# Optimization experiments

Measured on AMD Instinct MI355X. Metric: run time of the kernel, lower is better.

Reference implementation:

```python
import jax, jax.numpy as jnp
import numpy as np

NI = 256  # channels (c)
EPS = 1e-5  # BatchNorm eps


def setup_inputs() -> dict:
    key = jax.random.key(0)
    ks = jax.random.split(key, 7)
    n, c, h, w = 8, NI, 96, 96
    inp = jax.random.normal(ks[0], (n, c, h, w), dtype=jnp.float32)
    bn_gamma = jnp.ones((c,), dtype=jnp.float32)
    bn_beta = jnp.zeros((c,), dtype=jnp.float32)
    s_qkv = 1.0 / np.sqrt(c)
    w_qkv = jax.random.uniform(ks[1], (c, 3 * c), dtype=jnp.float32, minval=-s_qkv, maxval=s_qkv)
    b_qkv = jax.random.uniform(ks[2], (3 * c,), dtype=jnp.float32, minval=-s_qkv, maxval=s_qkv)
    w_proj = jax.random.uniform(ks[3], (c, c), dtype=jnp.float32, minval=-s_qkv, maxval=s_qkv)
    b_proj = jax.random.uniform(ks[4], (c,), dtype=jnp.float32, minval=-s_qkv, maxval=s_qkv)
    return {"inp": inp, "bn_gamma": bn_gamma, "bn_beta": bn_beta,
            "w_qkv": w_qkv, "b_qkv": b_qkv, "w_proj": w_proj, "b_proj": b_proj}


def reference(inp, bn_gamma, bn_beta, w_qkv, b_qkv, w_proj, b_proj):
    n, c, h, w = inp.shape
    # BatchNorm2d (training-mode batch statistics, biased variance)
    mean = jnp.mean(inp, axis=(0, 2, 3), keepdims=True)
    var = jnp.var(inp, axis=(0, 2, 3), keepdims=True)
    xn = (inp - mean) * jax.lax.rsqrt(var + EPS)
    xn = xn * bn_gamma.reshape(1, c, 1, 1) + bn_beta.reshape(1, c, 1, 1)
    # (n, c, h*w) -> (n, s, c)
    x = jnp.transpose(xn.reshape(n, c, h * w), (0, 2, 1))
    # fused QKV projection: (n, s, 3c)
    qkv = x @ w_qkv + b_qkv
    q, k, v = jnp.split(qkv, 3, axis=-1)  # each (n, s, c); nheads=1
    # linear attention: v + q @ (k^T @ v), avoids the (s, s) score matrix
    kv = jnp.einsum('nsd,nse->nde', k, v)        # (n, c, c)
    attn = v + jnp.einsum('nsd,nde->nse', q, kv)  # (n, s, c)
    # output projection (dropout is identity in eval mode)
    y = attn @ w_proj + b_proj                    # (n, s, c)
    y = jnp.transpose(y, (0, 2, 1)).reshape(n, c, h, w)
    return y + inp
```

## Files before the change

kernel.cpp:

```cpp
#include <hip/hip_runtime.h>
#include <hip/hip_bf16.h>
#include <stdint.h>

#define S 9216
#define C 256
#define NB 8
#define EPS 1e-5f

typedef __attribute__((ext_vector_type(8))) short bf16x8;
typedef __attribute__((ext_vector_type(4))) float f32x4;
typedef unsigned short u16;
typedef unsigned int u32;

#define WS_SC   0
#define WS_RX   4096
#define WS_DS   16384
#define WS_U    20480
#define WS_PV2  32768
#define WS_P1   45056
#define WS_PW   49152
#define WS_SHW  53248
#define WS_CZ   57344
#define WS_WKT  65536
#define WS_WPT  196608
#define WS_WPV  327680
#define WS_GB   458752
#define WS_T1   1507328
#define WS_AC2  2555904
#define WS_M    3604480
#define WS_XB   5242880
#define WS_XBT  42991616
#define WS_P    80740352

__device__ __forceinline__ float bf2f(u16 b) { return __uint_as_float((u32)b << 16); }
__device__ __forceinline__ u16 cvt1(float x) {
    __hip_bfloat16 h = __float2bfloat16(x);
    return *(u16*)&h;
}
__device__ __forceinline__ bf16x8 pack8(float4 a, float4 b) {
    union { bf16x8 v; u16 h[8]; } u;
    u.h[0] = cvt1(a.x); u.h[1] = cvt1(a.y); u.h[2] = cvt1(a.z); u.h[3] = cvt1(a.w);
    u.h[4] = cvt1(b.x); u.h[5] = cvt1(b.y); u.h[6] = cvt1(b.z); u.h[7] = cvt1(b.w);
    return u.v;
}
__device__ __forceinline__ void gl16(const u16* g, u16* l) {
    __builtin_amdgcn_global_load_lds(
        (const __attribute__((address_space(1))) unsigned int*)g,
        (__attribute__((address_space(3))) unsigned int*)l, 16, 0, 0);
}

__global__ __launch_bounds__(256)
void wt_build(const float* __restrict__ w_qkv, const float* __restrict__ w_proj,
              u16* __restrict__ wkT, u16* __restrict__ wpT) {
    const int r0 = blockIdx.x, c = threadIdx.x;
    if (r0 < 256) {
        wkT[(size_t)r0 * 256 + c] = cvt1(w_qkv[(size_t)c * 768 + 256 + r0]);
    } else {
        const int o = r0 - 256;
        wpT[(size_t)o * 256 + c] = cvt1(w_proj[(size_t)c * 256 + o]);
    }
}

__global__ __launch_bounds__(256)
void wpv_gemm(const u16* __restrict__ wpT, const float* __restrict__ w_qkv,
              u16* __restrict__ Wpv) {
    const int bid = blockIdx.x;
    const int ot = bid >> 2, ct = bid & 3;
    const int tid = threadIdx.x;
    const int w = tid >> 6, l = tid & 63, g = l >> 4, r = l & 15;
    const int wr = w >> 1, wc = w & 1;
    const int mb = ot * 64 + wr * 32, nb = ct * 64 + wc * 32;

    f32x4 acc[2][2];
    #pragma unroll
    for (int i = 0; i < 2; ++i)
        #pragma unroll
        for (int j = 0; j < 2; ++j) acc[i][j] = (f32x4){0.f, 0.f, 0.f, 0.f};

    for (int k0 = 0; k0 < 256; k0 += 32) {
        bf16x8 a[2], b[2];
        #pragma unroll
        for (int i = 0; i < 2; ++i)
            a[i] = *(const bf16x8*)&wpT[(size_t)(mb + i * 16 + r) * 256 + k0 + g * 8];
        #pragma unroll
        for (int j = 0; j < 2; ++j) {
            const float* p = w_qkv + (size_t)(nb + j * 16 + r) * 768 + 512 + k0 + g * 8;
            b[j] = pack8(*(const float4*)p, *(const float4*)(p + 4));
        }
        #pragma unroll
        for (int i = 0; i < 2; ++i)
            #pragma unroll
            for (int j = 0; j < 2; ++j)
                acc[i][j] = __builtin_amdgcn_mfma_f32_16x16x32_bf16(a[i], b[j], acc[i][j], 0, 0, 0);
    }
    #pragma unroll
    for (int i = 0; i < 2; ++i)
        #pragma unroll
        for (int q = 0; q < 4; ++q) {
            const int row = mb + i * 16 + g * 4 + q;
            #pragma unroll
            for (int j = 0; j < 2; ++j)
                Wpv[(size_t)row * 256 + nb + j * 16 + r] = cvt1(acc[i][j][q]);
        }
}

__global__ __launch_bounds__(256)
void cvt(const float* __restrict__ inp, u16* __restrict__ xb, u16* __restrict__ xbT,
         float* __restrict__ rx, float* __restrict__ diagS) {
    __shared__ u32 T32[64 * 129];
    const int bid = blockIdx.x;
    const int z = bid / 144, sb = bid % 144;
    const int s0 = sb * 64;
    const int t = threadIdx.x;
    const int l = t & 63, w = t >> 6;
    const int s4 = (l & 15) * 4, rq = l >> 4;
    const int odd = rq & 1;

    #pragma unroll
    for (int half = 0; half < 2; ++half) {
        float4 v[8];
        #pragma unroll
        for (int it = 0; it < 8; ++it) {
            const int row = (half * 8 + it) * 16 + w * 4 + rq;
            v[it] = *(const float4*)&inp[((size_t)(z * C + row)) * S + s0 + s4];
        }
        #pragma unroll
        for (int it = 0; it < 8; ++it) {
            const int row = (half * 8 + it) * 16 + w * 4 + rq;
            const size_t gidx = ((size_t)(z * C + row)) * S + s0 + s4;
            u16 b0 = cvt1(v[it].x), b1 = cvt1(v[it].y), b2 = cvt1(v[it].z), b3 = cvt1(v[it].w);
            u32 m01 = (u32)b0 | ((u32)b1 << 16);
            u32 m23 = (u32)b2 | ((u32)b3 << 16);
            uint2 pk; pk.x = m01; pk.y = m23;
            *(uint2*)&xb[gidx] = pk;
            u32 p01 = (u32)__shfl_xor((int)m01, 16, 64);
            u32 p23 = (u32)__shfl_xor((int)m23, 16, 64);
            u32 wA, wB;
            if (!odd) {
                wA = (m01 & 0xffffu) | ((p01 & 0xffffu) << 16);
                wB = (m01 >> 16) | (p01 & 0xffff0000u);
            } else {
                wA = (p23 & 0xffffu) | ((m23 & 0xffffu) << 16);
                wB = (p23 >> 16) | (m23 & 0xffff0000u);
            }
            const int row2 = row >> 1;
            const int su = s4 + odd * 2;
            T32[(su + 0) * 129 + row2] = wA;
            T32[(su + 1) * 129 + row2] = wB;
        }
    }
    __syncthreads();
    {
        const int cw = t >> 1, hi = t & 1;
        float sum = 0.f, ssq = 0.f;
        #pragma unroll 8
        for (int s = 0; s < 64; ++s) {
            u32 wv = T32[s * 129 + cw];
            float v = bf2f(hi ? (u16)(wv >> 16) : (u16)(wv & 0xffffu));
            sum += v; ssq = fmaf(v, v, ssq);
        }
        atomicAdd(&rx[z * 256 + t], sum);
        atomicAdd(&diagS[t], ssq);
    }
    const int sl = t >> 2, q4 = t & 3;
    u16* dst = xbT + ((size_t)z * S + s0 + sl) * 256 + q4 * 64;
    const u32* Trow = &T32[sl * 129 + q4 * 32];
    #pragma unroll
    for (int kk = 0; kk < 8; ++kk) {
        const int c0 = (kk * 4 + q4 * 8) & 31;
        uint4 q;
        q.x = Trow[c0 + 0]; q.y = Trow[c0 + 1];
        q.z = Trow[c0 + 2]; q.w = Trow[c0 + 3];
        *(uint4*)&dst[c0 * 2] = q;
    }
}

__global__ __launch_bounds__(256)
void bn_fin(const float* __restrict__ diagS, const float* __restrict__ rx,
            const float* __restrict__ gamma, const float* __restrict__ beta,
            float* __restrict__ sc_sh) {
    const int c = threadIdx.x;
    float s = 0.f;
    #pragma unroll
    for (int z = 0; z < NB; ++z) s += rx[z * 256 + c];
    const float q = diagS[c];
    const float invN = 1.0f / (float)(NB * S);
    float m = s * invN;
    float var = q * invN - m * m;
    float rstd = rsqrtf(var + EPS);
    float sc = gamma[c] * rstd;
    sc_sh[c] = sc;
    sc_sh[C + c] = beta[c] - m * sc;
}

__global__ __launch_bounds__(256)
void gram(const u16* __restrict__ xb, float* __restrict__ P) {
    __shared__ u16 Asm[128 * 32];
    __shared__ u16 Bsm[128 * 32];
    const int bid = blockIdx.x;
    const int wid = (bid & 7) * 96 + (bid >> 3);
    const int z = wid / 96;
    const int rem = wid % 96;
    const int tile = rem >> 5;
    const int sp = rem & 31;
    const int ti = (tile == 1) ? 1 : 0;
    const int tj = (tile == 0) ? 0 : 1;
    const bool diag = (tile < 2);

    const int t = threadIdx.x;
    const int w = t >> 6, l = t & 63, g = l >> 4, r = l & 15;
    const int wr = w >> 1, wc = w & 1;
    const int rsub = l >> 2, csub = (l & 3) * 8;

    const u16* Az = xb + (size_t)z * C * S;

    f32x4 acc[4][4];
    #pragma unroll
    for (int i = 0; i < 4; ++i)
        #pragma unroll
        for (int j = 0; j < 4; ++j) acc[i][j] = (f32x4){0.f, 0.f, 0.f, 0.f};

    const int sbeg = sp * 288;
    for (int k0 = 0; k0 < 288; k0 += 32) {
        const int sc = sbeg + k0 + csub;
        #pragma unroll
        for (int q = 0; q < 2; ++q) {
            const int ii = w * 2 + q;
            const int row16 = ii * 16 + rsub;
            gl16(Az + (size_t)(ti * 128 + row16) * S + sc, &Asm[ii * 512]);
            if (!diag)
                gl16(Az + (size_t)(tj * 128 + row16) * S + sc, &Bsm[ii * 512]);
        }
        __syncthreads();
        const u16* Bb = diag ? Asm : Bsm;
        bf16x8 a[4], b[4];
        #pragma unroll
        for (int i = 0; i < 4; ++i)
            a[i] = *(const bf16x8*)&Asm[(wr * 64 + i * 16 + r) * 32 + g * 8];
        #pragma unroll
        for (int j = 0; j < 4; ++j)
            b[j] = *(const bf16x8*)&Bb[(wc * 64 + j * 16 + r) * 32 + g * 8];
        #pragma unroll
        for (int i = 0; i < 4; ++i)
            #pragma unroll
            for (int j = 0; j < 4; ++j)
                acc[i][j] = __builtin_amdgcn_mfma_f32_16x16x32_bf16(a[i], b[j], acc[i][j], 0, 0, 0);
        __syncthreads();
    }
    float* PP = P + (((size_t)(z * 3 + tile) * 32 + sp) << 14);
    #pragma unroll
    for (int i = 0; i < 4; ++i)
        #pragma unroll
        for (int q = 0; q < 4; ++q) {
            const int row = wr * 64 + i * 16 + g * 4 + q;
            #pragma unroll
            for (int j = 0; j < 4; ++j)
                PP[row * 128 + wc * 64 + j * 16 + r] = acc[i][j][q];
        }
}

__global__ __launch_bounds__(256)
void g_red(const float* __restrict__ P, const float* __restrict__ rx,
           const float* __restrict__ sc_sh, u16* __restrict__ Gb) {
    __shared__ float scs[256], shs[256], rxl[256];
    __shared__ u16 TT[8][132];
    const int bid = blockIdx.x;
    const int z = bid / 48;
    const int rem = bid % 48;
    const int tile = rem >> 4;
    const int rc = rem & 15;
    const int ti = (tile == 1) ? 1 : 0;
    const int tj = (tile == 0) ? 0 : 1;
    const int t = threadIdx.x;
    scs[t] = sc_sh[t]; shs[t] = sc_sh[C + t]; rxl[t] = rx[z * 256 + t];
    __syncthreads();
    const int col = t & 127;
    const int r0 = t >> 7;
    const float* Pbase = P + (((size_t)(z * 3 + tile) * 32) << 14) + rc * 8 * 128 + col;
    u16* Gz = Gb + (size_t)z * 65536;
    #pragma unroll
    for (int k = 0; k < 4; ++k) {
        const int rl = r0 + k * 2;
        float s = 0.f;
        #pragma unroll 4
        for (int sp = 0; sp < 32; ++sp)
            s += Pbase[((size_t)sp << 14) + rl * 128];
        const int gr = ti * 128 + rc * 8 + rl;
        const int gc = tj * 128 + col;
        float v = scs[gr] * scs[gc] * s + scs[gr] * shs[gc] * rxl[gr]
                + shs[gr] * scs[gc] * rxl[gc] + 9216.f * shs[gr] * shs[gc];
        u16 o = cvt1(v);
        Gz[(size_t)gr * 256 + gc] = o;
        TT[rl][col] = o;
    }
    if (ti != tj) {
        __syncthreads();
        if (t < 128) {
            const int gc = tj * 128 + t;
            u16 o8[8];
            #pragma unroll
            for (int rl = 0; rl < 8; ++rl) o8[rl] = TT[rl][t];
            *(uint4*)&Gz[(size_t)gc * 256 + ti * 128 + rc * 8] = *(uint4*)o8;
        }
    }
}

__global__ __launch_bounds__(256)
void prep_v(const float* __restrict__ sc_sh, const float* __restrict__ rx,
            const u16* __restrict__ wkT, const u16* __restrict__ Wpv,
            const u16* __restrict__ wpT, const float* __restrict__ w_qkv,
            const float* __restrict__ b_qkv,
            float* __restrict__ uvec, float* __restrict__ pvec,
            float* __restrict__ p1, float* __restrict__ pw, float* __restrict__ shw) {
    const int z = blockIdx.x, t = threadIdx.x;
    __shared__ float rsn[256], bvl[256], shl[256];
    rsn[t] = sc_sh[t] * rx[z * 256 + t] + 9216.f * sc_sh[C + t];
    bvl[t] = b_qkv[512 + t];
    shl[t] = sc_sh[C + t];
    __syncthreads();
    float au = 0.f, ap = 0.f, apw = 0.f;
    const u16* krow = wkT + (size_t)t * 256;
    const u16* prow = Wpv + (size_t)t * 256;
    for (int cb = 0; cb < 256; cb += 8) {
        uint4 kp = *(const uint4*)&krow[cb];
        uint4 pp = *(const uint4*)&prow[cb];
        const u16* kk = (const u16*)&kp;
        const u16* qq = (const u16*)&pp;
        #pragma unroll
        for (int u = 0; u < 8; ++u) {
            au = fmaf(bf2f(kk[u]), rsn[cb + u], au);
            float pv = bf2f(qq[u]);
            ap = fmaf(pv, rsn[cb + u], ap);
            apw = fmaf(pv, shl[cb + u], apw);
        }
    }
    uvec[z * 256 + t] = au;
    pvec[z * 256 + t] = ap;
    if (z == 0) {
        float a1 = 0.f, asw = 0.f;
        const u16* wrow = wpT + (size_t)t * 256;
        for (int cb = 0; cb < 256; cb += 8) {
            uint4 wp = *(const uint4*)&wrow[cb];
            const u16* ww = (const u16*)&wp;
            #pragma unroll
            for (int u = 0; u < 8; ++u) a1 = fmaf(bf2f(ww[u]), bvl[cb + u], a1);
        }
        for (int c = 0; c < 256; ++c)
            asw = fmaf(w_qkv[(size_t)c * 768 + t], shl[c], asw);
        p1[t] = a1;
        pw[t] = apw;
        shw[t] = asw;
    }
}

__global__ __launch_bounds__(256)
void t1_gemm(const u16* __restrict__ Wpv, const u16* __restrict__ Gb,
             u16* __restrict__ T1) {
    const int bid = blockIdx.x;
    const int wid = (bid & 7) * 16 + (bid >> 3);
    const int z = wid >> 4, ot = (wid >> 2) & 3, ct = wid & 3;
    const int tid = threadIdx.x;
    const int w = tid >> 6, l = tid & 63, g = l >> 4, r = l & 15;
    const int wr = w >> 1, wc = w & 1;
    const int mb = ot * 64 + wr * 32, nb = ct * 64 + wc * 32;
    const u16* Gz = Gb + (size_t)z * 65536;

    f32x4 acc[2][2];
    #pragma unroll
    for (int i = 0; i < 2; ++i)
        #pragma unroll
        for (int j = 0; j < 2; ++j) acc[i][j] = (f32x4){0.f, 0.f, 0.f, 0.f};

    for (int k0 = 0; k0 < 256; k0 += 32) {
        bf16x8 a[2], b[2];
        #pragma unroll
        for (int i = 0; i < 2; ++i)
            a[i] = *(const bf16x8*)&Wpv[(size_t)(mb + i * 16 + r) * 256 + k0 + g * 8];
        #pragma unroll
        for (int j = 0; j < 2; ++j)
            b[j] = *(const bf16x8*)&Gz[(size_t)(nb + j * 16 + r) * 256 + k0 + g * 8];
        #pragma unroll
        for (int i = 0; i < 2; ++i)
            #pragma unroll
            for (int j = 0; j < 2; ++j)
                acc[i][j] = __builtin_amdgcn_mfma_f32_16x16x32_bf16(a[i], b[j], acc[i][j], 0, 0, 0);
    }
    u16* Tz = T1 + (size_t)z * 65536;
    #pragma unroll
    for (int i = 0; i < 2; ++i)
        #pragma unroll
        for (int q = 0; q < 4; ++q) {
            const int row = mb + i * 16 + g * 4 + q;
            #pragma unroll
            for (int j = 0; j < 2; ++j)
                Tz[(size_t)row * 256 + nb + j * 16 + r] = cvt1(acc[i][j][q]);
        }
}

__global__ __launch_bounds__(256)
void ac2_gemm(const u16* __restrict__ T1, const u16* __restrict__ wkT,
              const float* __restrict__ uvec, const float* __restrict__ pvec,
              const float* __restrict__ p1, const float* __restrict__ b_qkv,
              u16* __restrict__ Ac2) {
    const int bid = blockIdx.x;
    const int wid = (bid & 7) * 16 + (bid >> 3);
    const int z = wid >> 4, ot = (wid >> 2) & 3, ct = wid & 3;
    const int tid = threadIdx.x;
    const int w = tid >> 6, l = tid & 63, g = l >> 4, r = l & 15;
    const int wr = w >> 1, wc = w & 1;
    const int mb = ot * 64 + wr * 32, nb = ct * 64 + wc * 32;
    const u16* Tz = T1 + (size_t)z * 65536;

    f32x4 acc[2][2];
    #pragma unroll
    for (int i = 0; i < 2; ++i)
        #pragma unroll
        for (int j = 0; j < 2; ++j) acc[i][j] = (f32x4){0.f, 0.f, 0.f, 0.f};

    for (int k0 = 0; k0 < 256; k0 += 32) {
        bf16x8 a[2], b[2];
        #pragma unroll
        for (int i = 0; i < 2; ++i)
            a[i] = *(const bf16x8*)&Tz[(size_t)(mb + i * 16 + r) * 256 + k0 + g * 8];
        #pragma unroll
        for (int j = 0; j < 2; ++j)
            b[j] = *(const bf16x8*)&wkT[(size_t)(nb + j * 16 + r) * 256 + k0 + g * 8];
        #pragma unroll
        for (int i = 0; i < 2; ++i)
            #pragma unroll
            for (int j = 0; j < 2; ++j)
                acc[i][j] = __builtin_amdgcn_mfma_f32_16x16x32_bf16(a[i], b[j], acc[i][j], 0, 0, 0);
    }
    u16* Az = Ac2 + (size_t)z * 65536;
    #pragma unroll
    for (int i = 0; i < 2; ++i)
        #pragma unroll
        for (int q = 0; q < 4; ++q) {
            const int row = mb + i * 16 + g * 4 + q;
            const float p1r = p1[row];
            const float pvr = pvec[z * 256 + row];
            #pragma unroll
            for (int j = 0; j < 2; ++j) {
                const int col = nb + j * 16 + r;
                const float bkv = b_qkv[256 + col];
                const float uv = uvec[z * 256 + col];
                float v = acc[i][j][q] + p1r * (uv + 9216.f * bkv) + pvr * bkv;
                Az[(size_t)row * 256 + col] = cvt1(v);
            }
        }
}

__global__ __launch_bounds__(256)
void m_gemm(const u16* __restrict__ Ac2, const float* __restrict__ w_qkv,
            const u16* __restrict__ Wpv, const float* __restrict__ p1,
            const float* __restrict__ pw, const float* __restrict__ shw,
            const float* __restrict__ b_qkv, const float* __restrict__ b_proj,
            const float* __restrict__ sc_sh,
            u16* __restrict__ M, float* __restrict__ constz) {
    const int bid = blockIdx.x;
    const int wid = (bid & 7) * 16 + (bid >> 3);
    const int z = wid >> 4, ot = (wid >> 2) & 3, ct = wid & 3;
    const int tid = threadIdx.x;
    const int w = tid >> 6, l = tid & 63, g = l >> 4, r = l & 15;
    const int wr = w >> 1, wc = w & 1;
    const int mb = ot * 64 + wr * 32, nb = ct * 64 + wc * 32;
    const u16* Az = Ac2 + (size_t)z * 65536;
    const bool docz = (wc == 0 && ct == 0);

    f32x4 acc[2][2];
    #pragma unroll
    for (int i = 0; i < 2; ++i)
        #pragma unroll
        for (int j = 0; j < 2; ++j) acc[i][j] = (f32x4){0.f, 0.f, 0.f, 0.f};
    float cacc[2] = {0.f, 0.f};

    for (int k0 = 0; k0 < 256; k0 += 32) {
        bf16x8 a[2], b[2];
        #pragma unroll
        for (int i = 0; i < 2; ++i)
            a[i] = *(const bf16x8*)&Az[(size_t)(mb + i * 16 + r) * 256 + k0 + g * 8];
        #pragma unroll
        for (int j = 0; j < 2; ++j) {
            const float* p = w_qkv + (size_t)(nb + j * 16 + r) * 768 + k0 + g * 8;
            b[j] = pack8(*(const float4*)p, *(const float4*)(p + 4));
        }
        if (docz) {
            float bqv[8];
            #pragma unroll
            for (int u = 0; u < 8; ++u) {
                const int kg = k0 + g * 8 + u;
                bqv[u] = b_qkv[kg] + shw[kg];
            }
            #pragma unroll
            for (int i = 0; i < 2; ++i) {
                bf16x8 av = a[i];
                #pragma unroll
                for (int u = 0; u < 8; ++u)
                    cacc[i] = fmaf(bf2f((u16)av[u]), bqv[u], cacc[i]);
            }
        }
        #pragma unroll
        for (int i = 0; i < 2; ++i)
            #pragma unroll
            for (int j = 0; j < 2; ++j)
                acc[i][j] = __builtin_amdgcn_mfma_f32_16x16x32_bf16(a[i], b[j], acc[i][j], 0, 0, 0);
    }
    u16* Mz = M + (size_t)z * 65536;
    #pragma unroll
    for (int i = 0; i < 2; ++i)
        #pragma unroll
        for (int q = 0; q < 4; ++q) {
            const int row = mb + i * 16 + g * 4 + q;
            #pragma unroll
            for (int j = 0; j < 2; ++j) {
                const int col = nb + j * 16 + r;
                float v = acc[i][j][q] + bf2f(Wpv[(size_t)row * 256 + col]);
                Mz[(size_t)row * 256 + col] = cvt1(v * sc_sh[col]);
            }
        }
    if (docz) {
        #pragma unroll
        for (int i = 0; i < 2; ++i) {
            float rr2 = cacc[i];
            rr2 += __shfl_xor(rr2, 16, 64);
            rr2 += __shfl_xor(rr2, 32, 64);
            if (l < 16) {
                const int o = mb + i * 16 + l;
                constz[z * 256 + o] = b_proj[o] + p1[o] + pw[o] + rr2;
            }
        }
    }
}

__global__ __launch_bounds__(256)
void out_gemm(const u16* __restrict__ M, const u16* __restrict__ xbT,
              const float* __restrict__ inp, const float* __restrict__ constz,
              float* __restrict__ out) {
    __shared__ u16 Asm[128 * 32];
    __shared__ u16 Bsm[128 * 32];
    const int bid = blockIdx.x;
    const int wid = (bid & 7) * 144 + (bid >> 3);
    const int z = wid / 144;
    const int rem = wid % 144;
    const int ot = rem & 1, st = rem >> 1;

    const int t = threadIdx.x;
    const int l = t & 63, w = t >> 6;
    const int m0 = (w >> 1) * 64, n0 = (w & 1) * 64;
    const int g = l >> 4, r = l & 15;
    const int rsub = l >> 2, csub = (l & 3) * 8;

    const u16* Mz = M + (size_t)z * 65536;
    const u16* Bz = xbT + ((size_t)z * S + st * 128) * 256;

    f32x4 acc[4][4];
    #pragma unroll
    for (int i = 0; i < 4; ++i)
        #pragma unroll
        for (int j = 0; j < 4; ++j) acc[i][j] = (f32x4){0.f, 0.f, 0.f, 0.f};

    for (int k0 = 0; k0 < 256; k0 += 32) {
        #pragma unroll
        for (int q = 0; q < 2; ++q) {
            const int ii = w * 2 + q;
            const int row16 = ii * 16 + rsub;
            gl16(Mz + (size_t)(ot * 128 + row16) * 256 + k0 + csub, &Asm[ii * 512]);
            gl16(Bz + (size_t)row16 * 256 + k0 + csub, &Bsm[ii * 512]);
        }
        __syncthreads();
        bf16x8 a[4], b[4];
        #pragma unroll
        for (int i = 0; i < 4; ++i)
            a[i] = *(const bf16x8*)&Asm[(m0 + i * 16 + r) * 32 + g * 8];
        #pragma unroll
        for (int j = 0; j < 4; ++j)
            b[j] = *(const bf16x8*)&Bsm[(n0 + j * 16 + r) * 32 + g * 8];
        #pragma unroll
        for (int i = 0; i < 4; ++i)
            #pragma unroll
            for (int j = 0; j < 4; ++j)
                acc[i][j] = __builtin_amdgcn_mfma_f32_16x16x32_bf16(a[i], b[j], acc[i][j], 0, 0, 0);
        __syncthreads();
    }
    #pragma unroll
    for (int i = 0; i < 4; ++i) {
        #pragma unroll
        for (int q = 0; q < 4; ++q) {
            const int o = ot * 128 + m0 + i * 16 + g * 4 + q;
            const float cz = constz[z * 256 + o];
            const size_t base = ((size_t)(z * C + o)) * S + st * 128;
            #pragma unroll
            for (int j = 0; j < 4; ++j) {
                const int sl = n0 + j * 16 + r;
                out[base + sl] = acc[i][j][q] + cz + inp[base + sl];
            }
        }
    }
}

extern "C" void kernel_launch(void* const* d_in, const int* in_sizes, int n_in,
                              void* d_out, int out_size, void* d_ws, size_t ws_size,
                              hipStream_t stream) {
    const float* inp    = (const float*)d_in[0];
    const float* gamma  = (const float*)d_in[1];
    const float* beta   = (const float*)d_in[2];
    const float* w_qkv  = (const float*)d_in[3];
    const float* b_qkv  = (const float*)d_in[4];
    const float* w_proj = (const float*)d_in[5];
    const float* b_proj = (const float*)d_in[6];
    float* out = (float*)d_out;

    char* ws = (char*)d_ws;
    float* sc_sh = (float*)(ws + WS_SC);
    float* rx    = (float*)(ws + WS_RX);
    float* diagS = (float*)(ws + WS_DS);
    float* uvec  = (float*)(ws + WS_U);
    float* pvec  = (float*)(ws + WS_PV2);
    float* p1    = (float*)(ws + WS_P1);
    float* pw    = (float*)(ws + WS_PW);
    float* shw   = (float*)(ws + WS_SHW);
    float* cz    = (float*)(ws + WS_CZ);
    u16*   wkT   = (u16*)(ws + WS_WKT);
    u16*   wpT   = (u16*)(ws + WS_WPT);
    u16*   Wpv   = (u16*)(ws + WS_WPV);
    u16*   Gb    = (u16*)(ws + WS_GB);
    u16*   T1    = (u16*)(ws + WS_T1);
    u16*   Ac2   = (u16*)(ws + WS_AC2);
    u16*   Mm    = (u16*)(ws + WS_M);
    u16*   xb    = (u16*)(ws + WS_XB);
    u16*   xbT   = (u16*)(ws + WS_XBT);
    float* P     = (float*)(ws + WS_P);

    hipMemsetAsync(rx, 0, NB * 256 * sizeof(float), stream);
    hipMemsetAsync(diagS, 0, 256 * sizeof(float), stream);

    wt_build<<<dim3(512), dim3(256), 0, stream>>>(w_qkv, w_proj, wkT, wpT);
    wpv_gemm<<<dim3(16), dim3(256), 0, stream>>>(wpT, w_qkv, Wpv);
    cvt<<<dim3(1152), dim3(256), 0, stream>>>(inp, xb, xbT, rx, diagS);
    bn_fin<<<dim3(1), dim3(256), 0, stream>>>(diagS, rx, gamma, beta, sc_sh);
    gram<<<dim3(768), dim3(256), 0, stream>>>(xb, P);
    g_red<<<dim3(384), dim3(256), 0, stream>>>(P, rx, sc_sh, Gb);
    prep_v<<<dim3(NB), dim3(256), 0, stream>>>(sc_sh, rx, wkT, Wpv, wpT, w_qkv, b_qkv,
                                               uvec, pvec, p1, pw, shw);
    t1_gemm<<<dim3(128), dim3(256), 0, stream>>>(Wpv, Gb, T1);
    ac2_gemm<<<dim3(128), dim3(256), 0, stream>>>(T1, wkT, uvec, pvec, p1, b_qkv, Ac2);
    m_gemm<<<dim3(128), dim3(256), 0, stream>>>(Ac2, w_qkv, Wpv, p1, pw, shw,
                                                b_qkv, b_proj, sc_sh, Mm, cz);
    out_gemm<<<dim3(1152), dim3(256), 0, stream>>>(Mm, xbT, inp, cz, out);
}
```

Baseline: 176.7 us.

## Move BN stats to separate row-sum kernel and read bf16 residual

Removes the per-block atomic accumulation of channel sums and sums of squares from the conversion kernel. A new rsum kernel reduces each (batch, channel) row of the bf16 copy with wave shuffles and needs only one atomic per row. The conversion kernel now issues all 16 float4 loads up front instead of two batches of 8. The output GEMM reads the residual from the bf16 copy instead of the fp32 input, halving that traffic but adding bf16 rounding error to the residual, which could exceed tolerance.

```diff
diff --git a/kernel.cpp b/kernel.cpp
--- a/kernel.cpp
+++ b/kernel.cpp
@@ -105,8 +105,7 @@
 }
 
 __global__ __launch_bounds__(256)
-void cvt(const float* __restrict__ inp, u16* __restrict__ xb, u16* __restrict__ xbT,
-         float* __restrict__ rx, float* __restrict__ diagS) {
+void cvt(const float* __restrict__ inp, u16* __restrict__ xb, u16* __restrict__ xbT) {
     __shared__ u32 T32[64 * 129];
     const int bid = blockIdx.x;
     const int z = bid / 144, sb = bid % 144;
@@ -116,52 +115,37 @@
     const int s4 = (l & 15) * 4, rq = l >> 4;
     const int odd = rq & 1;
 
-    #pragma unroll
-    for (int half = 0; half < 2; ++half) {
-        float4 v[8];
-        #pragma unroll
-        for (int it = 0; it < 8; ++it) {
-            const int row = (half * 8 + it) * 16 + w * 4 + rq;
-            v[it] = *(const float4*)&inp[((size_t)(z * C + row)) * S + s0 + s4];
-        }
-        #pragma unroll
-        for (int it = 0; it < 8; ++it) {
-            const int row = (half * 8 + it) * 16 + w * 4 + rq;
-            const size_t gidx = ((size_t)(z * C + row)) * S + s0 + s4;
-            u16 b0 = cvt1(v[it].x), b1 = cvt1(v[it].y), b2 = cvt1(v[it].z), b3 = cvt1(v[it].w);
-            u32 m01 = (u32)b0 | ((u32)b1 << 16);
-            u32 m23 = (u32)b2 | ((u32)b3 << 16);
-            uint2 pk; pk.x = m01; pk.y = m23;
-            *(uint2*)&xb[gidx] = pk;
-            u32 p01 = (u32)__shfl_xor((int)m01, 16, 64);
-            u32 p23 = (u32)__shfl_xor((int)m23, 16, 64);
-            u32 wA, wB;
-            if (!odd) {
-                wA = (m01 & 0xffffu) | ((p01 & 0xffffu) << 16);
-                wB = (m01 >> 16) | (p01 & 0xffff0000u);
-            } else {
-                wA = (p23 & 0xffffu) | ((m23 & 0xffffu) << 16);
-                wB = (p23 >> 16) | (m23 & 0xffff0000u);
-            }
-            const int row2 = row >> 1;
-            const int su = s4 + odd * 2;
-            T32[(su + 0) * 129 + row2] = wA;
-            T32[(su + 1) * 129 + row2] = wB;
-        }
+    float4 v[16];
+    #pragma unroll
+    for (int it = 0; it < 16; ++it) {
+        const int row = it * 16 + w * 4 + rq;
+        v[it] = *(const float4*)&inp[((size_t)(z * C + row)) * S + s0 + s4];
+    }
+    #pragma unroll
+    for (int it = 0; it < 16; ++it) {
+        const int row = it * 16 + w * 4 + rq;
+        const size_t gidx = ((size_t)(z * C + row)) * S + s0 + s4;
+        u16 b0 = cvt1(v[it].x), b1 = cvt1(v[it].y), b2 = cvt1(v[it].z), b3 = cvt1(v[it].w);
+        u32 m01 = (u32)b0 | ((u32)b1 << 16);
+        u32 m23 = (u32)b2 | ((u32)b3 << 16);
+        uint2 pk; pk.x = m01; pk.y = m23;
+        *(uint2*)&xb[gidx] = pk;
+        u32 p01 = (u32)__shfl_xor((int)m01, 16, 64);
+        u32 p23 = (u32)__shfl_xor((int)m23, 16, 64);
+        u32 wA, wB;
+        if (!odd) {
+            wA = (m01 & 0xffffu) | ((p01 & 0xffffu) << 16);
+            wB = (m01 >> 16) | (p01 & 0xffff0000u);
+        } else {
+            wA = (p23 & 0xffffu) | ((m23 & 0xffffu) << 16);
+            wB = (p23 >> 16) | (m23 & 0xffff0000u);
+        }
+        const int row2 = row >> 1;
+        const int su = s4 + odd * 2;
+        T32[(su + 0) * 129 + row2] = wA;
+        T32[(su + 1) * 129 + row2] = wB;
     }
     __syncthreads();
-    {
-        const int cw = t >> 1, hi = t & 1;
-        float sum = 0.f, ssq = 0.f;
-        #pragma unroll 8
-        for (int s = 0; s < 64; ++s) {
-            u32 wv = T32[s * 129 + cw];
-            float v = bf2f(hi ? (u16)(wv >> 16) : (u16)(wv & 0xffffu));
-            sum += v; ssq = fmaf(v, v, ssq);
-        }
-        atomicAdd(&rx[z * 256 + t], sum);
-        atomicAdd(&diagS[t], ssq);
-    }
     const int sl = t >> 2, q4 = t & 3;
     u16* dst = xbT + ((size_t)z * S + s0 + sl) * 256 + q4 * 64;
     const u32* Trow = &T32[sl * 129 + q4 * 32];
@@ -172,6 +156,39 @@
         q.x = Trow[c0 + 0]; q.y = Trow[c0 + 1];
         q.z = Trow[c0 + 2]; q.w = Trow[c0 + 3];
         *(uint4*)&dst[c0 * 2] = q;
+    }
+}
+
+__global__ __launch_bounds__(256)
+void rsum(const u16* __restrict__ xb, float* __restrict__ rx, float* __restrict__ diagS) {
+    const int row = blockIdx.x;
+    const int t = threadIdx.x;
+    const uint4* p = (const uint4*)(xb + (size_t)row * S);
+    float sum = 0.f, ssq = 0.f;
+    for (int i = t; i < 1152; i += 256) {
+        uint4 v = p[i];
+        const u32 wv[4] = {v.x, v.y, v.z, v.w};
+        #pragma unroll
+        for (int k = 0; k < 4; ++k) {
+            float a = bf2f((u16)(wv[k] & 0xffffu));
+            float b = bf2f((u16)(wv[k] >> 16));
+            sum += a + b;
+            ssq = fmaf(a, a, ssq);
+            ssq = fmaf(b, b, ssq);
+        }
+    }
+    #pragma unroll
+    for (int off = 32; off > 0; off >>= 1) {
+        sum += __shfl_down(sum, off, 64);
+        ssq += __shfl_down(ssq, off, 64);
+    }
+    __shared__ float sred[8];
+    const int wv2 = t >> 6, ln = t & 63;
+    if (ln == 0) { sred[wv2] = sum; sred[4 + wv2] = ssq; }
+    __syncthreads();
+    if (t == 0) {
+        rx[row] = sred[0] + sred[1] + sred[2] + sred[3];
+        atomicAdd(&diagS[row & 255], sred[4] + sred[5] + sred[6] + sred[7]);
     }
 }
 
@@ -534,7 +551,7 @@
 
 __global__ __launch_bounds__(256)
 void out_gemm(const u16* __restrict__ M, const u16* __restrict__ xbT,
-              const float* __restrict__ inp, const float* __restrict__ constz,
+              const u16* __restrict__ xb, const float* __restrict__ constz,
               float* __restrict__ out) {
     __shared__ u16 Asm[128 * 32];
     __shared__ u16 Bsm[128 * 32];
@@ -592,7 +609,7 @@
             #pragma unroll
             for (int j = 0; j < 4; ++j) {
                 const int sl = n0 + j * 16 + r;
-                out[base + sl] = acc[i][j][q] + cz + inp[base + sl];
+                out[base + sl] = acc[i][j][q] + cz + bf2f(xb[base + sl]);
             }
         }
     }
@@ -631,12 +648,12 @@
     u16*   xbT   = (u16*)(ws + WS_XBT);
     float* P     = (float*)(ws + WS_P);
 
-    hipMemsetAsync(rx, 0, NB * 256 * sizeof(float), stream);
     hipMemsetAsync(diagS, 0, 256 * sizeof(float), stream);
 
     wt_build<<<dim3(512), dim3(256), 0, stream>>>(w_qkv, w_proj, wkT, wpT);
     wpv_gemm<<<dim3(16), dim3(256), 0, stream>>>(wpT, w_qkv, Wpv);
-    cvt<<<dim3(1152), dim3(256), 0, stream>>>(inp, xb, xbT, rx, diagS);
+    cvt<<<dim3(1152), dim3(256), 0, stream>>>(inp, xb, xbT);
+    rsum<<<dim3(2048), dim3(256), 0, stream>>>(xb, rx, diagS);
     bn_fin<<<dim3(1), dim3(256), 0, stream>>>(diagS, rx, gamma, beta, sc_sh);
     gram<<<dim3(768), dim3(256), 0, stream>>>(xb, P);
     g_red<<<dim3(384), dim3(256), 0, stream>>>(P, rx, sc_sh, Gb);
@@ -646,5 +663,5 @@
     ac2_gemm<<<dim3(128), dim3(256), 0, stream>>>(T1, wkT, uvec, pvec, p1, b_qkv, Ac2);
     m_gemm<<<dim3(128), dim3(256), 0, stream>>>(Ac2, w_qkv, Wpv, p1, pw, shw,
                                                 b_qkv, b_proj, sc_sh, Mm, cz);
-    out_gemm<<<dim3(1152), dim3(256), 0, stream>>>(Mm, xbT, inp, cz, out);
-}
+    out_gemm<<<dim3(1152), dim3(256), 0, stream>>>(Mm, xbT, xb, cz, out);
+}
```

New measurement: 180.0 us. Within noise of the previous version (+1.9%).

## Double-buffer LDS in gram and out_gemm, read residual from bf16 copy

Applied to the files above, without the earlier changes.

The gram and out_gemm kernels now keep two LDS stages, so the next k-slice is fetched while MFMAs run on the current one. The cvt kernel issues all 16 float4 loads before converting, which raises memory-level parallelism. out_gemm now reads the residual from the bf16 copy of the input instead of the fp32 tensor, which halves that read traffic. The cost is doubled LDS use per block and a loss of precision in the residual add.

```diff
diff --git a/kernel.cpp b/kernel.cpp
--- a/kernel.cpp
+++ b/kernel.cpp
@@ -116,38 +116,35 @@
     const int s4 = (l & 15) * 4, rq = l >> 4;
     const int odd = rq & 1;
 
-    #pragma unroll
-    for (int half = 0; half < 2; ++half) {
-        float4 v[8];
-        #pragma unroll
-        for (int it = 0; it < 8; ++it) {
-            const int row = (half * 8 + it) * 16 + w * 4 + rq;
-            v[it] = *(const float4*)&inp[((size_t)(z * C + row)) * S + s0 + s4];
-        }
-        #pragma unroll
-        for (int it = 0; it < 8; ++it) {
-            const int row = (half * 8 + it) * 16 + w * 4 + rq;
-            const size_t gidx = ((size_t)(z * C + row)) * S + s0 + s4;
-            u16 b0 = cvt1(v[it].x), b1 = cvt1(v[it].y), b2 = cvt1(v[it].z), b3 = cvt1(v[it].w);
-            u32 m01 = (u32)b0 | ((u32)b1 << 16);
-            u32 m23 = (u32)b2 | ((u32)b3 << 16);
-            uint2 pk; pk.x = m01; pk.y = m23;
-            *(uint2*)&xb[gidx] = pk;
-            u32 p01 = (u32)__shfl_xor((int)m01, 16, 64);
-            u32 p23 = (u32)__shfl_xor((int)m23, 16, 64);
-            u32 wA, wB;
-            if (!odd) {
-                wA = (m01 & 0xffffu) | ((p01 & 0xffffu) << 16);
-                wB = (m01 >> 16) | (p01 & 0xffff0000u);
-            } else {
-                wA = (p23 & 0xffffu) | ((m23 & 0xffffu) << 16);
-                wB = (p23 >> 16) | (m23 & 0xffff0000u);
-            }
-            const int row2 = row >> 1;
-            const int su = s4 + odd * 2;
-            T32[(su + 0) * 129 + row2] = wA;
-            T32[(su + 1) * 129 + row2] = wB;
-        }
+    float4 v[16];
+    #pragma unroll
+    for (int it = 0; it < 16; ++it) {
+        const int row = it * 16 + w * 4 + rq;
+        v[it] = *(const float4*)&inp[((size_t)(z * C + row)) * S + s0 + s4];
+    }
+    #pragma unroll
+    for (int it = 0; it < 16; ++it) {
+        const int row = it * 16 + w * 4 + rq;
+        const size_t gidx = ((size_t)(z * C + row)) * S + s0 + s4;
+        u16 b0 = cvt1(v[it].x), b1 = cvt1(v[it].y), b2 = cvt1(v[it].z), b3 = cvt1(v[it].w);
+        u32 m01 = (u32)b0 | ((u32)b1 << 16);
+        u32 m23 = (u32)b2 | ((u32)b3 << 16);
+        uint2 pk; pk.x = m01; pk.y = m23;
+        *(uint2*)&xb[gidx] = pk;
+        u32 p01 = (u32)__shfl_xor((int)m01, 16, 64);
+        u32 p23 = (u32)__shfl_xor((int)m23, 16, 64);
+        u32 wA, wB;
+        if (!odd) {
+            wA = (m01 & 0xffffu) | ((p01 & 0xffffu) << 16);
+            wB = (m01 >> 16) | (p01 & 0xffff0000u);
+        } else {
+            wA = (p23 & 0xffffu) | ((m23 & 0xffffu) << 16);
+            wB = (p23 >> 16) | (m23 & 0xffff0000u);
+        }
+        const int row2 = row >> 1;
+        const int su = s4 + odd * 2;
+        T32[(su + 0) * 129 + row2] = wA;
+        T32[(su + 1) * 129 + row2] = wB;
     }
     __syncthreads();
     {
@@ -156,8 +153,8 @@
         #pragma unroll 8
         for (int s = 0; s < 64; ++s) {
             u32 wv = T32[s * 129 + cw];
-            float v = bf2f(hi ? (u16)(wv >> 16) : (u16)(wv & 0xffffu));
-            sum += v; ssq = fmaf(v, v, ssq);
+            float vv = bf2f(hi ? (u16)(wv >> 16) : (u16)(wv & 0xffffu));
+            sum += vv; ssq = fmaf(vv, vv, ssq);
         }
         atomicAdd(&rx[z * 256 + t], sum);
         atomicAdd(&diagS[t], ssq);
@@ -195,8 +192,8 @@
 
 __global__ __launch_bounds__(256)
 void gram(const u16* __restrict__ xb, float* __restrict__ P) {
-    __shared__ u16 Asm[128 * 32];
-    __shared__ u16 Bsm[128 * 32];
+    __shared__ u16 Asm[2][128 * 32];
+    __shared__ u16 Bsm[2][128 * 32];
     const int bid = blockIdx.x;
     const int wid = (bid & 7) * 96 + (bid >> 3);
     const int z = wid / 96;
@@ -213,6 +210,7 @@
     const int rsub = l >> 2, csub = (l & 3) * 8;
 
     const u16* Az = xb + (size_t)z * C * S;
+    const int sbeg = sp * 288;
 
     f32x4 acc[4][4];
     #pragma unroll
@@ -220,23 +218,37 @@
         #pragma unroll
         for (int j = 0; j < 4; ++j) acc[i][j] = (f32x4){0.f, 0.f, 0.f, 0.f};
 
-    const int sbeg = sp * 288;
-    for (int k0 = 0; k0 < 288; k0 += 32) {
-        const int sc = sbeg + k0 + csub;
+    {
+        const int sc = sbeg + csub;
         #pragma unroll
         for (int q = 0; q < 2; ++q) {
             const int ii = w * 2 + q;
             const int row16 = ii * 16 + rsub;
-            gl16(Az + (size_t)(ti * 128 + row16) * S + sc, &Asm[ii * 512]);
+            gl16(Az + (size_t)(ti * 128 + row16) * S + sc, &Asm[0][ii * 512]);
             if (!diag)
-                gl16(Az + (size_t)(tj * 128 + row16) * S + sc, &Bsm[ii * 512]);
-        }
-        __syncthreads();
-        const u16* Bb = diag ? Asm : Bsm;
+                gl16(Az + (size_t)(tj * 128 + row16) * S + sc, &Bsm[0][ii * 512]);
+        }
+    }
+    __syncthreads();
+
+    for (int k0 = 0; k0 < 288; k0 += 32) {
+        const int cur = (k0 >> 5) & 1;
+        if (k0 + 32 < 288) {
+            const int sc = sbeg + k0 + 32 + csub;
+            #pragma unroll
+            for (int q = 0; q < 2; ++q) {
+                const int ii = w * 2 + q;
+                const int row16 = ii * 16 + rsub;
+                gl16(Az + (size_t)(ti * 128 + row16) * S + sc, &Asm[cur ^ 1][ii * 512]);
+                if (!diag)
+                    gl16(Az + (size_t)(tj * 128 + row16) * S + sc, &Bsm[cur ^ 1][ii * 512]);
+            }
+        }
+        const u16* Bb = diag ? Asm[cur] : Bsm[cur];
         bf16x8 a[4], b[4];
         #pragma unroll
         for (int i = 0; i < 4; ++i)
-            a[i] = *(const bf16x8*)&Asm[(wr * 64 + i * 16 + r) * 32 + g * 8];
+            a[i] = *(const bf16x8*)&Asm[cur][(wr * 64 + i * 16 + r) * 32 + g * 8];
         #pragma unroll
         for (int j = 0; j < 4; ++j)
             b[j] = *(const bf16x8*)&Bb[(wc * 64 + j * 16 + r) * 32 + g * 8];
@@ -534,10 +546,10 @@
 
 __global__ __launch_bounds__(256)
 void out_gemm(const u16* __restrict__ M, const u16* __restrict__ xbT,
-              const float* __restrict__ inp, const float* __restrict__ constz,
+              const u16* __restrict__ xb, const float* __restrict__ constz,
               float* __restrict__ out) {
-    __shared__ u16 Asm[128 * 32];
-    __shared__ u16 Bsm[128 * 32];
+    __shared__ u16 Asm[2][128 * 32];
+    __shared__ u16 Bsm[2][128 * 32];
     const int bid = blockIdx.x;
     const int wid = (bid & 7) * 144 + (bid >> 3);
     const int z = wid / 144;
@@ -559,22 +571,33 @@
         #pragma unroll
         for (int j = 0; j < 4; ++j) acc[i][j] = (f32x4){0.f, 0.f, 0.f, 0.f};
 
+    #pragma unroll
+    for (int q = 0; q < 2; ++q) {
+        const int ii = w * 2 + q;
+        const int row16 = ii * 16 + rsub;
+        gl16(Mz + (size_t)(ot * 128 + row16) * 256 + csub, &Asm[0][ii * 512]);
+        gl16(Bz + (size_t)row16 * 256 + csub, &Bsm[0][ii * 512]);
+    }
+    __syncthreads();
+
     for (int k0 = 0; k0 < 256; k0 += 32) {
-        #pragma unroll
-        for (int q = 0; q < 2; ++q) {
-            const int ii = w * 2 + q;
-            const int row16 = ii * 16 + rsub;
-            gl16(Mz + (size_t)(ot * 128 + row16) * 256 + k0 + csub, &Asm[ii * 512]);
-            gl16(Bz + (size_t)row16 * 256 + k0 + csub, &Bsm[ii * 512]);
-        }
-        __syncthreads();
+        const int cur = (k0 >> 5) & 1;
+        if (k0 < 224) {
+            #pragma unroll
+            for (int q = 0; q < 2; ++q) {
+                const int ii = w * 2 + q;
+                const int row16 = ii * 16 + rsub;
+                gl16(Mz + (size_t)(ot * 128 + row16) * 256 + k0 + 32 + csub, &Asm[cur ^ 1][ii * 512]);
+                gl16(Bz + (size_t)row16 * 256 + k0 + 32 + csub, &Bsm[cur ^ 1][ii * 512]);
+            }
+        }
         bf16x8 a[4], b[4];
         #pragma unroll
         for (int i = 0; i < 4; ++i)
-            a[i] = *(const bf16x8*)&Asm[(m0 + i * 16 + r) * 32 + g * 8];
+            a[i] = *(const bf16x8*)&Asm[cur][(m0 + i * 16 + r) * 32 + g * 8];
         #pragma unroll
         for (int j = 0; j < 4; ++j)
-            b[j] = *(const bf16x8*)&Bsm[(n0 + j * 16 + r) * 32 + g * 8];
+            b[j] = *(const bf16x8*)&Bsm[cur][(n0 + j * 16 + r) * 32 + g * 8];
         #pragma unroll
         for (int i = 0; i < 4; ++i)
             #pragma unroll
@@ -592,7 +615,7 @@
             #pragma unroll
             for (int j = 0; j < 4; ++j) {
                 const int sl = n0 + j * 16 + r;
-                out[base + sl] = acc[i][j][q] + cz + inp[base + sl];
+                out[base + sl] = acc[i][j][q] + cz + bf2f(xb[base + sl]);
             }
         }
     }
@@ -646,5 +669,5 @@
     ac2_gemm<<<dim3(128), dim3(256), 0, stream>>>(T1, wkT, uvec, pvec, p1, b_qkv, Ac2);
     m_gemm<<<dim3(128), dim3(256), 0, stream>>>(Ac2, w_qkv, Wpv, p1, pw, shw,
                                                 b_qkv, b_proj, sc_sh, Mm, cz);
-    out_gemm<<<dim3(1152), dim3(256), 0, stream>>>(Mm, xbT, inp, cz, out);
-}
+    out_gemm<<<dim3(1152), dim3(256), 0, stream>>>(Mm, xbT, xb, cz, out);
+}
```

Result: slower. 187.2 us (+5.9%).
